# Kernel tuning notes

Hardware: AMD Instinct MI355X
Metric: run time of the kernel (lower is better)

The kernel has to match this reference:

```python
import jax, jax.numpy as jnp
import numpy as np

P = 8192          # pool_size
D = 4096          # input_dim
B = 4             # batch
SPARSITY = 0.1
NC = int(P * P * SPARSITY)  # 6710886 COO nonzeros


def setup_inputs() -> dict:
    key = jax.random.key(0)
    ks = jax.random.split(key, 5)
    return {
        "x": jax.random.normal(ks[0], (B, D), dtype=jnp.float32),
        "W_proj": jax.random.normal(ks[1], (P, D), dtype=jnp.float32) / np.float32(np.sqrt(D)),
        "b_proj": jnp.zeros((P,), dtype=jnp.float32),
        "conn_values": jax.random.normal(ks[2], (NC,), dtype=jnp.float32) * 0.1,
        "sparse_state": jnp.zeros((P,), dtype=jnp.float32),
        "conn_rows": jax.random.randint(ks[3], (NC,), 0, P, dtype=jnp.int32),
        "conn_cols": jax.random.randint(ks[4], (NC,), 0, P, dtype=jnp.int32),
    }


def reference(x, W_proj, b_proj, conn_values, sparse_state, conn_rows, conn_cols):
    # input projection: [B, D] @ [D, P] -> [B, P]
    a = x @ W_proj.T + b_proj
    # quantile threshold over all elements of |a| (matches torch.quantile on full tensor)
    thr = jnp.quantile(jnp.abs(a), 1.0 - SPARSITY)
    mask = jnp.abs(a) > thr                     # [B, P]
    # decay old state, then overwrite active entries with row-0 activation
    a0, m0 = a[0], mask[0]                      # [P], [P]
    state = jnp.where(m0, a0, sparse_state * 0.9)
    # sparse COO matvec: recurrent[r] += v * state[c] for each nonzero (r, c, v)
    contrib = conn_values * state[conn_cols]    # [NC]
    recurrent = jax.ops.segment_sum(contrib, conn_rows, num_segments=P)
    # fused state update + exact GELU (torch nn.GELU default)
    new_state = jax.nn.gelu(state + 0.1 * recurrent, approximate=False)
    # BoundedAttractorState scalars
    active_count = m0.sum()
    mean_activity = jnp.where(
        active_count > 0,
        jnp.sum(jnp.where(m0, new_state, 0.0)) / jnp.maximum(active_count, 1).astype(new_state.dtype),
        0.0,
    )
    return new_state, active_count, mean_activity
```

## Files before the change

### kernel.cpp

```cpp
#include <hip/hip_runtime.h>
#include <math.h>

#define PP 8192
#define DD 4096
#define BBATCH 4
#define NTOT (BBATCH * PP)
#define K_LOW 29490
#define NBINS 8192
#define SCALE 1048576.0f
#define INV_SCALE (1.0f / 1048576.0f)
#define LIST_CAP 3072

__device__ __forceinline__ float dot4(float4 w, float4 v) {
  return fmaf(w.x, v.x, fmaf(w.y, v.y, fmaf(w.z, v.z, w.w * v.w)));
}

__global__ __launch_bounds__(256, 4) void gemm_kernel(const float* __restrict__ x,
                                                      const float* __restrict__ W,
                                                      const float* __restrict__ bias,
                                                      float* __restrict__ a,
                                                      unsigned* __restrict__ hist,
                                                      int* __restrict__ rec) {
  if (blockIdx.x < 32) {
    hist[blockIdx.x * 256 + threadIdx.x] = 0u;
  } else if (blockIdx.x < 64) {
    rec[(blockIdx.x - 32) * 256 + threadIdx.x] = 0;
  }
  const int wave = threadIdx.x >> 6;
  const int lane = threadIdx.x & 63;
  const int p0 = blockIdx.x * 8 + wave * 2;
  const float4* __restrict__ W0 = (const float4*)(W + (size_t)p0 * DD);
  const float4* __restrict__ W1 = W0 + (DD / 4);
  const float4* __restrict__ x4 = (const float4*)x;
  double a00 = 0.0, a01 = 0.0, a02 = 0.0, a03 = 0.0;
  double a10 = 0.0, a11 = 0.0, a12 = 0.0, a13 = 0.0;
  #pragma unroll 4
  for (int k = 0; k < 16; ++k) {
    const int i = lane + k * 64;
    float4 w0 = W0[i];
    float4 w1 = W1[i];
    float4 v0 = x4[i];
    float4 v1 = x4[1024 + i];
    float4 v2 = x4[2048 + i];
    float4 v3 = x4[3072 + i];
    a00 += (double)dot4(w0, v0);
    a01 += (double)dot4(w0, v1);
    a02 += (double)dot4(w0, v2);
    a03 += (double)dot4(w0, v3);
    a10 += (double)dot4(w1, v0);
    a11 += (double)dot4(w1, v1);
    a12 += (double)dot4(w1, v2);
    a13 += (double)dot4(w1, v3);
  }
  #pragma unroll
  for (int off = 32; off > 0; off >>= 1) {
    a00 += __shfl_down(a00, off);
    a01 += __shfl_down(a01, off);
    a02 += __shfl_down(a02, off);
    a03 += __shfl_down(a03, off);
    a10 += __shfl_down(a10, off);
    a11 += __shfl_down(a11, off);
    a12 += __shfl_down(a12, off);
    a13 += __shfl_down(a13, off);
  }
  if (lane == 0) {
    float b0 = bias[p0];
    float b1 = bias[p0 + 1];
    a[0 * PP + p0] = (float)a00 + b0;
    a[1 * PP + p0] = (float)a01 + b0;
    a[2 * PP + p0] = (float)a02 + b0;
    a[3 * PP + p0] = (float)a03 + b0;
    a[0 * PP + p0 + 1] = (float)a10 + b1;
    a[1 * PP + p0 + 1] = (float)a11 + b1;
    a[2 * PP + p0 + 1] = (float)a12 + b1;
    a[3 * PP + p0 + 1] = (float)a13 + b1;
  }
}

__global__ __launch_bounds__(1024) void hist_kernel(const float* __restrict__ a,
                                                    unsigned* __restrict__ hist) {
  __shared__ unsigned h[NBINS];
  const int tid = threadIdx.x;
  #pragma unroll
  for (int j = 0; j < NBINS / 1024; ++j) h[tid + j * 1024] = 0u;
  __syncthreads();
  const int base = blockIdx.x * 4096 + tid;
  #pragma unroll
  for (int k = 0; k < 4; ++k) {
    unsigned u = __float_as_uint(fabsf(a[base + k * 1024]));
    atomicAdd(&h[u >> 18], 1u);
  }
  __syncthreads();
  #pragma unroll
  for (int j = 0; j < NBINS / 1024; ++j) {
    unsigned c = h[tid + j * 1024];
    if (c) atomicAdd(&hist[tid + j * 1024], c);
  }
}

__global__ __launch_bounds__(1024) void thr_kernel(const float* __restrict__ a,
                                                   const unsigned* __restrict__ hist,
                                                   float* __restrict__ thr) {
  __shared__ unsigned scan[1024];
  __shared__ unsigned list1[LIST_CAP];
  __shared__ unsigned list2[LIST_CAP];
  __shared__ unsigned s_n1, s_n2;
  __shared__ unsigned s_b1, s_r1, s_b2, s_r2;
  __shared__ unsigned s_vlo, s_vhi;
  const int tid = threadIdx.x;
  const uint4* h4 = (const uint4*)hist;
  uint4 q0 = h4[tid * 2];
  uint4 q1 = h4[tid * 2 + 1];
  unsigned part = q0.x + q0.y + q0.z + q0.w + q1.x + q1.y + q1.z + q1.w;
  scan[tid] = part;
  if (tid == 0) { s_n1 = 0; s_n2 = 0; }
  __syncthreads();
  for (int off = 1; off < 1024; off <<= 1) {
    unsigned v = (tid >= off) ? scan[tid - off] : 0u;
    __syncthreads();
    scan[tid] += v;
    __syncthreads();
  }
  const unsigned incl = scan[tid];
  const unsigned excl = incl - part;
  unsigned bins[8] = {q0.x, q0.y, q0.z, q0.w, q1.x, q1.y, q1.z, q1.w};
  if (excl <= (unsigned)K_LOW && (unsigned)K_LOW < incl) {
    unsigned r = (unsigned)K_LOW - excl, cum = 0;
    #pragma unroll
    for (int j = 0; j < 8; ++j) {
      if (cum + bins[j] > r) { s_b1 = tid * 8 + j; s_r1 = r - cum; break; }
      cum += bins[j];
    }
  }
  if (excl <= (unsigned)(K_LOW + 1) && (unsigned)(K_LOW + 1) < incl) {
    unsigned r = (unsigned)(K_LOW + 1) - excl, cum = 0;
    #pragma unroll
    for (int j = 0; j < 8; ++j) {
      if (cum + bins[j] > r) { s_b2 = tid * 8 + j; s_r2 = r - cum; break; }
      cum += bins[j];
    }
  }
  __syncthreads();
  const unsigned b1 = s_b1, r1 = s_r1, b2 = s_b2, r2 = s_r2;
  for (int i = tid; i < NTOT; i += 1024) {
    unsigned u = __float_as_uint(fabsf(a[i]));
    unsigned bk = u >> 18;
    if (bk == b1) {
      unsigned idx = atomicAdd(&s_n1, 1u);
      if (idx < LIST_CAP) list1[idx] = u;
    } else if (bk == b2) {
      unsigned idx = atomicAdd(&s_n2, 1u);
      if (idx < LIST_CAP) list2[idx] = u;
    }
  }
  __syncthreads();
  const unsigned m1 = min(s_n1, (unsigned)LIST_CAP);
  const unsigned m2 = min(s_n2, (unsigned)LIST_CAP);
  for (unsigned i = tid; i < m1; i += 1024) {
    unsigned ui = list1[i];
    unsigned ltc = 0, eqb = 0;
    for (unsigned j = 0; j < m1; ++j) {
      unsigned uj = list1[j];
      ltc += (uj < ui) ? 1u : 0u;
      eqb += ((uj == ui) && (j < i)) ? 1u : 0u;
    }
    unsigned rk = ltc + eqb;
    if (rk == r1) s_vlo = ui;
    if (b2 == b1 && rk == r2) s_vhi = ui;
  }
  if (b2 != b1) {
    for (unsigned i = tid; i < m2; i += 1024) {
      unsigned ui = list2[i];
      unsigned ltc = 0, eqb = 0;
      for (unsigned j = 0; j < m2; ++j) {
        unsigned uj = list2[j];
        ltc += (uj < ui) ? 1u : 0u;
        eqb += ((uj == ui) && (j < i)) ? 1u : 0u;
      }
      if (ltc + eqb == r2) s_vhi = ui;
    }
  }
  __syncthreads();
  if (tid == 0) {
    double dlo = (double)__uint_as_float(s_vlo);
    double dhi = (double)__uint_as_float(s_vhi);
    double idx = 0.9 * (double)(NTOT - 1);
    double g = idx - floor(idx);
    thr[0] = (float)(dlo + g * (dhi - dlo));
  }
}

__global__ __launch_bounds__(1024) void spmv_kernel(const float* __restrict__ vals,
                                                    const int* __restrict__ rows,
                                                    const int* __restrict__ cols,
                                                    const float* __restrict__ a,
                                                    const float* __restrict__ thr,
                                                    const float* __restrict__ sstate,
                                                    int* __restrict__ rec,
                                                    int nc) {
  __shared__ float s_state[PP];
  __shared__ int s_rec[PP];
  const int tid = threadIdx.x;
  const float t = thr[0];
  for (int i = tid; i < PP; i += 1024) {
    float a0 = a[i];
    s_state[i] = (fabsf(a0) > t) ? a0 : 0.9f * sstate[i];
    s_rec[i] = 0;
  }
  __syncthreads();
  const int n4 = nc >> 2;
  const int stride = gridDim.x * 1024;
  const float4* __restrict__ v4 = (const float4*)vals;
  const int4* __restrict__ r4 = (const int4*)rows;
  const int4* __restrict__ c4 = (const int4*)cols;
  for (int i = blockIdx.x * 1024 + tid; i < n4; i += stride) {
    float4 v = v4[i];
    int4 r = r4[i];
    int4 c = c4[i];
    atomicAdd((unsigned*)&s_rec[r.x], (unsigned)__float2int_rn(v.x * s_state[c.x] * SCALE));
    atomicAdd((unsigned*)&s_rec[r.y], (unsigned)__float2int_rn(v.y * s_state[c.y] * SCALE));
    atomicAdd((unsigned*)&s_rec[r.z], (unsigned)__float2int_rn(v.z * s_state[c.z] * SCALE));
    atomicAdd((unsigned*)&s_rec[r.w], (unsigned)__float2int_rn(v.w * s_state[c.w] * SCALE));
  }
  if (blockIdx.x == 0 && tid < (nc - (n4 << 2))) {
    int i = (n4 << 2) + tid;
    atomicAdd((unsigned*)&s_rec[rows[i]],
              (unsigned)__float2int_rn(vals[i] * s_state[cols[i]] * SCALE));
  }
  __syncthreads();
  for (int i = tid; i < PP; i += 1024)
    atomicAdd((unsigned*)&rec[i], (unsigned)s_rec[i]);
}

__global__ __launch_bounds__(256) void reduce_gelu_kernel(const int* __restrict__ rec,
                                                          const float* __restrict__ a,
                                                          const float* __restrict__ thr,
                                                          const float* __restrict__ sstate,
                                                          float* __restrict__ out) {
  const int p = blockIdx.x * 256 + threadIdx.x;
  float r = (float)rec[p] * INV_SCALE;
  float a0 = a[p];
  float t = thr[0];
  float st = (fabsf(a0) > t) ? a0 : 0.9f * sstate[p];
  float v = st + 0.1f * r;
  out[p] = 0.5f * v * (1.0f + erff(v * 0.70710678118654752440f));
}

__global__ __launch_bounds__(1024) void scalars_kernel(const float* __restrict__ a,
                                                       const float* __restrict__ thr,
                                                       const float* __restrict__ out_state,
                                                       float* __restrict__ out) {
  __shared__ float wsum[16];
  __shared__ unsigned wcnt[16];
  const float t = thr[0];
  float lsum = 0.0f;
  unsigned lcnt = 0;
  for (int p = threadIdx.x; p < PP; p += 1024) {
    if (fabsf(a[p]) > t) { lsum += out_state[p]; lcnt++; }
  }
  #pragma unroll
  for (int off = 32; off > 0; off >>= 1) {
    lsum += __shfl_down(lsum, off);
    lcnt += __shfl_down(lcnt, off);
  }
  const int lane = threadIdx.x & 63;
  const int wid = threadIdx.x >> 6;
  if (lane == 0) { wsum[wid] = lsum; wcnt[wid] = lcnt; }
  __syncthreads();
  if (threadIdx.x == 0) {
    float s = 0.0f;
    unsigned c = 0;
    for (int w = 0; w < 16; ++w) { s += wsum[w]; c += wcnt[w]; }
    out[PP] = (float)c;
    out[PP + 1] = (c > 0) ? (s / (float)c) : 0.0f;
  }
}

extern "C" void kernel_launch(void* const* d_in, const int* in_sizes, int n_in,
                              void* d_out, int out_size, void* d_ws, size_t ws_size,
                              hipStream_t stream) {
  const float* x      = (const float*)d_in[0];
  const float* W      = (const float*)d_in[1];
  const float* bias   = (const float*)d_in[2];
  const float* vals   = (const float*)d_in[3];
  const float* sstate = (const float*)d_in[4];
  const int*   rows   = (const int*)d_in[5];
  const int*   cols   = (const int*)d_in[6];
  const int    nc     = in_sizes[3];
  float* out = (float*)d_out;
  float* ws  = (float*)d_ws;

  float*    a    = ws;
  float*    thr  = ws + 32768;
  unsigned* hist = (unsigned*)(ws + 32784);
  int*      rec  = (int*)(ws + 32784 + NBINS);

  gemm_kernel<<<PP / 8, 256, 0, stream>>>(x, W, bias, a, hist, rec);
  hist_kernel<<<NTOT / 4096, 1024, 0, stream>>>(a, hist);
  thr_kernel<<<1, 1024, 0, stream>>>(a, hist, thr);
  spmv_kernel<<<256, 1024, 0, stream>>>(vals, rows, cols, a, thr, sstate, rec, nc);
  reduce_gelu_kernel<<<PP / 256, 256, 0, stream>>>(rec, a, thr, sstate, out);
  scalars_kernel<<<1, 1024, 0, stream>>>(a, thr, out, out);
}
```

Before: 82.19 us.

## Fuse histogram into threshold kernel, scalars into GELU, widen GEMM row tile

Removes the multi-block histogram kernel by having the single-block threshold kernel build the histogram in shared memory directly. The scalars reduction is fused into the GELU finalize kernel using fixed-point atomics and a last-block-done counter. The GEMM now computes four rows per wave instead of two, halving the grid. Together these cut two launches, at the cost of a serial 32K-element histogram pass in one block and fixed-point rounding of the mean.

```diff
diff --git a/kernel.cpp b/kernel.cpp
--- a/kernel.cpp
+++ b/kernel.cpp
@@ -3,12 +3,13 @@
 
 #define PP 8192
 #define DD 4096
-#define BBATCH 4
-#define NTOT (BBATCH * PP)
+#define NTOT 32768
 #define K_LOW 29490
 #define NBINS 8192
 #define SCALE 1048576.0f
 #define INV_SCALE (1.0f / 1048576.0f)
+#define MSCALE 262144.0f
+#define INV_MSCALE (1.0f / 262144.0f)
 #define LIST_CAP 3072
 
 __device__ __forceinline__ float dot4(float4 w, float4 v) {
@@ -19,88 +20,75 @@
                                                       const float* __restrict__ W,
                                                       const float* __restrict__ bias,
                                                       float* __restrict__ a,
-                                                      unsigned* __restrict__ hist,
-                                                      int* __restrict__ rec) {
+                                                      int* __restrict__ rec,
+                                                      int* __restrict__ acc) {
   if (blockIdx.x < 32) {
-    hist[blockIdx.x * 256 + threadIdx.x] = 0u;
-  } else if (blockIdx.x < 64) {
-    rec[(blockIdx.x - 32) * 256 + threadIdx.x] = 0;
+    rec[blockIdx.x * 256 + threadIdx.x] = 0;
+  } else if (blockIdx.x == 32 && threadIdx.x < 4) {
+    acc[threadIdx.x] = 0;
   }
   const int wave = threadIdx.x >> 6;
   const int lane = threadIdx.x & 63;
-  const int p0 = blockIdx.x * 8 + wave * 2;
-  const float4* __restrict__ W0 = (const float4*)(W + (size_t)p0 * DD);
-  const float4* __restrict__ W1 = W0 + (DD / 4);
+  const int p0 = blockIdx.x * 16 + wave * 4;
+  const float4* __restrict__ Wr[4];
+  #pragma unroll
+  for (int r = 0; r < 4; ++r) Wr[r] = (const float4*)(W + (size_t)(p0 + r) * DD);
   const float4* __restrict__ x4 = (const float4*)x;
-  double a00 = 0.0, a01 = 0.0, a02 = 0.0, a03 = 0.0;
-  double a10 = 0.0, a11 = 0.0, a12 = 0.0, a13 = 0.0;
-  #pragma unroll 4
+  double accd[4][4];
+  #pragma unroll
+  for (int r = 0; r < 4; ++r)
+    #pragma unroll
+    for (int b = 0; b < 4; ++b) accd[r][b] = 0.0;
+  #pragma unroll 2
   for (int k = 0; k < 16; ++k) {
     const int i = lane + k * 64;
-    float4 w0 = W0[i];
-    float4 w1 = W1[i];
+    float4 w0 = Wr[0][i];
+    float4 w1 = Wr[1][i];
+    float4 w2 = Wr[2][i];
+    float4 w3 = Wr[3][i];
     float4 v0 = x4[i];
     float4 v1 = x4[1024 + i];
     float4 v2 = x4[2048 + i];
     float4 v3 = x4[3072 + i];
-    a00 += (double)dot4(w0, v0);
-    a01 += (double)dot4(w0, v1);
-    a02 += (double)dot4(w0, v2);
-    a03 += (double)dot4(w0, v3);
-    a10 += (double)dot4(w1, v0);
-    a11 += (double)dot4(w1, v1);
-    a12 += (double)dot4(w1, v2);
-    a13 += (double)dot4(w1, v3);
-  }
-  #pragma unroll
-  for (int off = 32; off > 0; off >>= 1) {
-    a00 += __shfl_down(a00, off);
-    a01 += __shfl_down(a01, off);
-    a02 += __shfl_down(a02, off);
-    a03 += __shfl_down(a03, off);
-    a10 += __shfl_down(a10, off);
-    a11 += __shfl_down(a11, off);
-    a12 += __shfl_down(a12, off);
-    a13 += __shfl_down(a13, off);
+    accd[0][0] += (double)dot4(w0, v0);
+    accd[0][1] += (double)dot4(w0, v1);
+    accd[0][2] += (double)dot4(w0, v2);
+    accd[0][3] += (double)dot4(w0, v3);
+    accd[1][0] += (double)dot4(w1, v0);
+    accd[1][1] += (double)dot4(w1, v1);
+    accd[1][2] += (double)dot4(w1, v2);
+    accd[1][3] += (double)dot4(w1, v3);
+    accd[2][0] += (double)dot4(w2, v0);
+    accd[2][1] += (double)dot4(w2, v1);
+    accd[2][2] += (double)dot4(w2, v2);
+    accd[2][3] += (double)dot4(w2, v3);
+    accd[3][0] += (double)dot4(w3, v0);
+    accd[3][1] += (double)dot4(w3, v1);
+    accd[3][2] += (double)dot4(w3, v2);
+    accd[3][3] += (double)dot4(w3, v3);
+  }
+  #pragma unroll
+  for (int r = 0; r < 4; ++r)
+    #pragma unroll
+    for (int b = 0; b < 4; ++b)
+      #pragma unroll
+      for (int off = 32; off > 0; off >>= 1)
+        accd[r][b] += __shfl_down(accd[r][b], off);
+  if (lane < 4) {
   }
   if (lane == 0) {
-    float b0 = bias[p0];
-    float b1 = bias[p0 + 1];
-    a[0 * PP + p0] = (float)a00 + b0;
-    a[1 * PP + p0] = (float)a01 + b0;
-    a[2 * PP + p0] = (float)a02 + b0;
-    a[3 * PP + p0] = (float)a03 + b0;
-    a[0 * PP + p0 + 1] = (float)a10 + b1;
-    a[1 * PP + p0 + 1] = (float)a11 + b1;
-    a[2 * PP + p0 + 1] = (float)a12 + b1;
-    a[3 * PP + p0 + 1] = (float)a13 + b1;
-  }
-}
-
-__global__ __launch_bounds__(1024) void hist_kernel(const float* __restrict__ a,
-                                                    unsigned* __restrict__ hist) {
+    #pragma unroll
+    for (int r = 0; r < 4; ++r) {
+      float bp = bias[p0 + r];
+      #pragma unroll
+      for (int b = 0; b < 4; ++b) a[b * PP + p0 + r] = (float)accd[r][b] + bp;
+    }
+  }
+}
+
+__global__ __launch_bounds__(1024) void thr_kernel(const float* __restrict__ a,
+                                                   float* __restrict__ thr) {
   __shared__ unsigned h[NBINS];
-  const int tid = threadIdx.x;
-  #pragma unroll
-  for (int j = 0; j < NBINS / 1024; ++j) h[tid + j * 1024] = 0u;
-  __syncthreads();
-  const int base = blockIdx.x * 4096 + tid;
-  #pragma unroll
-  for (int k = 0; k < 4; ++k) {
-    unsigned u = __float_as_uint(fabsf(a[base + k * 1024]));
-    atomicAdd(&h[u >> 18], 1u);
-  }
-  __syncthreads();
-  #pragma unroll
-  for (int j = 0; j < NBINS / 1024; ++j) {
-    unsigned c = h[tid + j * 1024];
-    if (c) atomicAdd(&hist[tid + j * 1024], c);
-  }
-}
-
-__global__ __launch_bounds__(1024) void thr_kernel(const float* __restrict__ a,
-                                                   const unsigned* __restrict__ hist,
-                                                   float* __restrict__ thr) {
   __shared__ unsigned scan[1024];
   __shared__ unsigned list1[LIST_CAP];
   __shared__ unsigned list2[LIST_CAP];
@@ -108,12 +96,22 @@
   __shared__ unsigned s_b1, s_r1, s_b2, s_r2;
   __shared__ unsigned s_vlo, s_vhi;
   const int tid = threadIdx.x;
-  const uint4* h4 = (const uint4*)hist;
-  uint4 q0 = h4[tid * 2];
-  uint4 q1 = h4[tid * 2 + 1];
-  unsigned part = q0.x + q0.y + q0.z + q0.w + q1.x + q1.y + q1.z + q1.w;
+  #pragma unroll
+  for (int j = 0; j < NBINS / 1024; ++j) h[tid + j * 1024] = 0u;
+  if (tid == 0) { s_n1 = 0; s_n2 = 0; }
+  __syncthreads();
+  for (int i = tid; i < NTOT; i += 1024) {
+    unsigned u = __float_as_uint(fabsf(a[i]));
+    atomicAdd(&h[u >> 18], 1u);
+  }
+  __syncthreads();
+  unsigned bins[8];
+  #pragma unroll
+  for (int j = 0; j < 8; ++j) bins[j] = h[tid * 8 + j];
+  unsigned part = 0;
+  #pragma unroll
+  for (int j = 0; j < 8; ++j) part += bins[j];
   scan[tid] = part;
-  if (tid == 0) { s_n1 = 0; s_n2 = 0; }
   __syncthreads();
   for (int off = 1; off < 1024; off <<= 1) {
     unsigned v = (tid >= off) ? scan[tid - off] : 0u;
@@ -123,7 +121,6 @@
   }
   const unsigned incl = scan[tid];
   const unsigned excl = incl - part;
-  unsigned bins[8] = {q0.x, q0.y, q0.z, q0.w, q1.x, q1.y, q1.z, q1.w};
   if (excl <= (unsigned)K_LOW && (unsigned)K_LOW < incl) {
     unsigned r = (unsigned)K_LOW - excl, cum = 0;
     #pragma unroll
@@ -232,32 +229,25 @@
     atomicAdd((unsigned*)&rec[i], (unsigned)s_rec[i]);
 }
 
-__global__ __launch_bounds__(256) void reduce_gelu_kernel(const int* __restrict__ rec,
-                                                          const float* __restrict__ a,
-                                                          const float* __restrict__ thr,
-                                                          const float* __restrict__ sstate,
-                                                          float* __restrict__ out) {
+__global__ __launch_bounds__(256) void finalize_kernel(const int* __restrict__ rec,
+                                                       const float* __restrict__ a,
+                                                       const float* __restrict__ thr,
+                                                       const float* __restrict__ sstate,
+                                                       float* __restrict__ out,
+                                                       int* __restrict__ acc) {
+  __shared__ float wsum[4];
+  __shared__ unsigned wcnt[4];
   const int p = blockIdx.x * 256 + threadIdx.x;
+  const float t = thr[0];
   float r = (float)rec[p] * INV_SCALE;
   float a0 = a[p];
-  float t = thr[0];
   float st = (fabsf(a0) > t) ? a0 : 0.9f * sstate[p];
   float v = st + 0.1f * r;
-  out[p] = 0.5f * v * (1.0f + erff(v * 0.70710678118654752440f));
-}
-
-__global__ __launch_bounds__(1024) void scalars_kernel(const float* __restrict__ a,
-                                                       const float* __restrict__ thr,
-                                                       const float* __restrict__ out_state,
-                                                       float* __restrict__ out) {
-  __shared__ float wsum[16];
-  __shared__ unsigned wcnt[16];
-  const float t = thr[0];
-  float lsum = 0.0f;
-  unsigned lcnt = 0;
-  for (int p = threadIdx.x; p < PP; p += 1024) {
-    if (fabsf(a[p]) > t) { lsum += out_state[p]; lcnt++; }
-  }
+  float ns = 0.5f * v * (1.0f + erff(v * 0.70710678118654752440f));
+  out[p] = ns;
+  bool m = fabsf(a0) > t;
+  float lsum = m ? ns : 0.0f;
+  unsigned lcnt = m ? 1u : 0u;
   #pragma unroll
   for (int off = 32; off > 0; off >>= 1) {
     lsum += __shfl_down(lsum, off);
@@ -268,11 +258,18 @@
   if (lane == 0) { wsum[wid] = lsum; wcnt[wid] = lcnt; }
   __syncthreads();
   if (threadIdx.x == 0) {
-    float s = 0.0f;
-    unsigned c = 0;
-    for (int w = 0; w < 16; ++w) { s += wsum[w]; c += wcnt[w]; }
-    out[PP] = (float)c;
-    out[PP + 1] = (c > 0) ? (s / (float)c) : 0.0f;
+    float bsum = wsum[0] + wsum[1] + wsum[2] + wsum[3];
+    unsigned bcnt = wcnt[0] + wcnt[1] + wcnt[2] + wcnt[3];
+    atomicAdd((unsigned*)&acc[0], (unsigned)__float2int_rn(bsum * MSCALE));
+    atomicAdd((unsigned*)&acc[1], bcnt);
+    __threadfence();
+    unsigned d = atomicAdd((unsigned*)&acc[2], 1u);
+    if (d == (unsigned)(gridDim.x - 1)) {
+      int sfix = atomicAdd(&acc[0], 0);
+      int cnt = atomicAdd(&acc[1], 0);
+      out[PP] = (float)cnt;
+      out[PP + 1] = (cnt > 0) ? ((float)sfix * INV_MSCALE / (float)cnt) : 0.0f;
+    }
   }
 }
 
@@ -290,15 +287,13 @@
   float* out = (float*)d_out;
   float* ws  = (float*)d_ws;
 
-  float*    a    = ws;
-  float*    thr  = ws + 32768;
-  unsigned* hist = (unsigned*)(ws + 32784);
-  int*      rec  = (int*)(ws + 32784 + NBINS);
-
-  gemm_kernel<<<PP / 8, 256, 0, stream>>>(x, W, bias, a, hist, rec);
-  hist_kernel<<<NTOT / 4096, 1024, 0, stream>>>(a, hist);
-  thr_kernel<<<1, 1024, 0, stream>>>(a, hist, thr);
+  float* a   = ws;
+  float* thr = ws + 32768;
+  int*   rec = (int*)(ws + 32784);
+  int*   acc = (int*)(ws + 32784 + PP);
+
+  gemm_kernel<<<PP / 16, 256, 0, stream>>>(x, W, bias, a, rec, acc);
+  thr_kernel<<<1, 1024, 0, stream>>>(a, thr);
   spmv_kernel<<<256, 1024, 0, stream>>>(vals, rows, cols, a, thr, sstate, rec, nc);
-  reduce_gelu_kernel<<<PP / 256, 256, 0, stream>>>(rec, a, thr, sstate, out);
-  scalars_kernel<<<1, 1024, 0, stream>>>(a, thr, out, out);
-}
+  finalize_kernel<<<PP / 256, 256, 0, stream>>>(rec, a, thr, sstate, out, acc);
+}
```

Measured after the change: 85.06 us. +3.5%, slower.

## Fuse histogram into GEMM epilogue and merge GELU with scalar reduction

Applied to the files above, without the earlier changes.

The histogram of |a| is now built with global atomics in the GEMM epilogue, which removes the separate hist kernel. The GELU kernel and the single-block scalars kernel are merged into one finalize kernel. It does a last-block-done reduction using fixed-point atomics for the sum. Zeroing of hist, rec and acc moves from GEMM blocks to a hipMemsetAsync. This cuts two kernel launches and one reread of a. In exchange it adds contended global atomics on the histogram and a fixed-point approximation of the mean sum.

```diff
diff --git a/kernel.cpp b/kernel.cpp
--- a/kernel.cpp
+++ b/kernel.cpp
@@ -3,12 +3,13 @@
 
 #define PP 8192
 #define DD 4096
-#define BBATCH 4
-#define NTOT (BBATCH * PP)
+#define NTOT 32768
 #define K_LOW 29490
 #define NBINS 8192
 #define SCALE 1048576.0f
 #define INV_SCALE (1.0f / 1048576.0f)
+#define MSCALE 262144.0f
+#define INV_MSCALE (1.0f / 262144.0f)
 #define LIST_CAP 3072
 
 __device__ __forceinline__ float dot4(float4 w, float4 v) {
@@ -19,13 +20,7 @@
                                                       const float* __restrict__ W,
                                                       const float* __restrict__ bias,
                                                       float* __restrict__ a,
-                                                      unsigned* __restrict__ hist,
-                                                      int* __restrict__ rec) {
-  if (blockIdx.x < 32) {
-    hist[blockIdx.x * 256 + threadIdx.x] = 0u;
-  } else if (blockIdx.x < 64) {
-    rec[(blockIdx.x - 32) * 256 + threadIdx.x] = 0;
-  }
+                                                      unsigned* __restrict__ hist) {
   const int wave = threadIdx.x >> 6;
   const int lane = threadIdx.x & 63;
   const int p0 = blockIdx.x * 8 + wave * 2;
@@ -66,35 +61,30 @@
   if (lane == 0) {
     float b0 = bias[p0];
     float b1 = bias[p0 + 1];
-    a[0 * PP + p0] = (float)a00 + b0;
-    a[1 * PP + p0] = (float)a01 + b0;
-    a[2 * PP + p0] = (float)a02 + b0;
-    a[3 * PP + p0] = (float)a03 + b0;
-    a[0 * PP + p0 + 1] = (float)a10 + b1;
-    a[1 * PP + p0 + 1] = (float)a11 + b1;
-    a[2 * PP + p0 + 1] = (float)a12 + b1;
-    a[3 * PP + p0 + 1] = (float)a13 + b1;
-  }
-}
-
-__global__ __launch_bounds__(1024) void hist_kernel(const float* __restrict__ a,
-                                                    unsigned* __restrict__ hist) {
-  __shared__ unsigned h[NBINS];
-  const int tid = threadIdx.x;
-  #pragma unroll
-  for (int j = 0; j < NBINS / 1024; ++j) h[tid + j * 1024] = 0u;
-  __syncthreads();
-  const int base = blockIdx.x * 4096 + tid;
-  #pragma unroll
-  for (int k = 0; k < 4; ++k) {
-    unsigned u = __float_as_uint(fabsf(a[base + k * 1024]));
-    atomicAdd(&h[u >> 18], 1u);
-  }
-  __syncthreads();
-  #pragma unroll
-  for (int j = 0; j < NBINS / 1024; ++j) {
-    unsigned c = h[tid + j * 1024];
-    if (c) atomicAdd(&hist[tid + j * 1024], c);
+    float r00 = (float)a00 + b0;
+    float r01 = (float)a01 + b0;
+    float r02 = (float)a02 + b0;
+    float r03 = (float)a03 + b0;
+    float r10 = (float)a10 + b1;
+    float r11 = (float)a11 + b1;
+    float r12 = (float)a12 + b1;
+    float r13 = (float)a13 + b1;
+    a[0 * PP + p0] = r00;
+    a[1 * PP + p0] = r01;
+    a[2 * PP + p0] = r02;
+    a[3 * PP + p0] = r03;
+    a[0 * PP + p0 + 1] = r10;
+    a[1 * PP + p0 + 1] = r11;
+    a[2 * PP + p0 + 1] = r12;
+    a[3 * PP + p0 + 1] = r13;
+    atomicAdd(&hist[__float_as_uint(fabsf(r00)) >> 18], 1u);
+    atomicAdd(&hist[__float_as_uint(fabsf(r01)) >> 18], 1u);
+    atomicAdd(&hist[__float_as_uint(fabsf(r02)) >> 18], 1u);
+    atomicAdd(&hist[__float_as_uint(fabsf(r03)) >> 18], 1u);
+    atomicAdd(&hist[__float_as_uint(fabsf(r10)) >> 18], 1u);
+    atomicAdd(&hist[__float_as_uint(fabsf(r11)) >> 18], 1u);
+    atomicAdd(&hist[__float_as_uint(fabsf(r12)) >> 18], 1u);
+    atomicAdd(&hist[__float_as_uint(fabsf(r13)) >> 18], 1u);
   }
 }
 
@@ -232,32 +222,25 @@
     atomicAdd((unsigned*)&rec[i], (unsigned)s_rec[i]);
 }
 
-__global__ __launch_bounds__(256) void reduce_gelu_kernel(const int* __restrict__ rec,
-                                                          const float* __restrict__ a,
-                                                          const float* __restrict__ thr,
-                                                          const float* __restrict__ sstate,
-                                                          float* __restrict__ out) {
+__global__ __launch_bounds__(256) void finalize_kernel(const int* __restrict__ rec,
+                                                       const float* __restrict__ a,
+                                                       const float* __restrict__ thr,
+                                                       const float* __restrict__ sstate,
+                                                       float* __restrict__ out,
+                                                       int* __restrict__ acc) {
+  __shared__ float wsum[4];
+  __shared__ unsigned wcnt[4];
   const int p = blockIdx.x * 256 + threadIdx.x;
+  const float t = thr[0];
   float r = (float)rec[p] * INV_SCALE;
   float a0 = a[p];
-  float t = thr[0];
-  float st = (fabsf(a0) > t) ? a0 : 0.9f * sstate[p];
+  bool m = fabsf(a0) > t;
+  float st = m ? a0 : 0.9f * sstate[p];
   float v = st + 0.1f * r;
-  out[p] = 0.5f * v * (1.0f + erff(v * 0.70710678118654752440f));
-}
-
-__global__ __launch_bounds__(1024) void scalars_kernel(const float* __restrict__ a,
-                                                       const float* __restrict__ thr,
-                                                       const float* __restrict__ out_state,
-                                                       float* __restrict__ out) {
-  __shared__ float wsum[16];
-  __shared__ unsigned wcnt[16];
-  const float t = thr[0];
-  float lsum = 0.0f;
-  unsigned lcnt = 0;
-  for (int p = threadIdx.x; p < PP; p += 1024) {
-    if (fabsf(a[p]) > t) { lsum += out_state[p]; lcnt++; }
-  }
+  float ns = 0.5f * v * (1.0f + erff(v * 0.70710678118654752440f));
+  out[p] = ns;
+  float lsum = m ? ns : 0.0f;
+  unsigned lcnt = m ? 1u : 0u;
   #pragma unroll
   for (int off = 32; off > 0; off >>= 1) {
     lsum += __shfl_down(lsum, off);
@@ -268,11 +251,18 @@
   if (lane == 0) { wsum[wid] = lsum; wcnt[wid] = lcnt; }
   __syncthreads();
   if (threadIdx.x == 0) {
-    float s = 0.0f;
-    unsigned c = 0;
-    for (int w = 0; w < 16; ++w) { s += wsum[w]; c += wcnt[w]; }
-    out[PP] = (float)c;
-    out[PP + 1] = (c > 0) ? (s / (float)c) : 0.0f;
+    float bsum = wsum[0] + wsum[1] + wsum[2] + wsum[3];
+    unsigned bcnt = wcnt[0] + wcnt[1] + wcnt[2] + wcnt[3];
+    atomicAdd((unsigned*)&acc[0], (unsigned)__float2int_rn(bsum * MSCALE));
+    atomicAdd((unsigned*)&acc[1], bcnt);
+    __threadfence();
+    unsigned d = atomicAdd((unsigned*)&acc[2], 1u);
+    if (d == (unsigned)(gridDim.x - 1)) {
+      int sfix = (int)atomicAdd((unsigned*)&acc[0], 0u);
+      int cnt = (int)atomicAdd((unsigned*)&acc[1], 0u);
+      out[PP] = (float)cnt;
+      out[PP + 1] = (cnt > 0) ? ((float)sfix * INV_MSCALE / (float)cnt) : 0.0f;
+    }
   }
 }
 
@@ -294,11 +284,11 @@
   float*    thr  = ws + 32768;
   unsigned* hist = (unsigned*)(ws + 32784);
   int*      rec  = (int*)(ws + 32784 + NBINS);
-
-  gemm_kernel<<<PP / 8, 256, 0, stream>>>(x, W, bias, a, hist, rec);
-  hist_kernel<<<NTOT / 4096, 1024, 0, stream>>>(a, hist);
+  int*      acc  = (int*)(ws + 32784 + NBINS + PP);
+
+  hipMemsetAsync(hist, 0, (NBINS + PP + 4) * sizeof(unsigned), stream);
+  gemm_kernel<<<PP / 8, 256, 0, stream>>>(x, W, bias, a, hist);
   thr_kernel<<<1, 1024, 0, stream>>>(a, hist, thr);
   spmv_kernel<<<256, 1024, 0, stream>>>(vals, rows, cols, a, thr, sstate, rec, nc);
-  reduce_gelu_kernel<<<PP / 256, 256, 0, stream>>>(rec, a, thr, sstate, out);
-  scalars_kernel<<<1, 1024, 0, stream>>>(a, thr, out, out);
-}
+  finalize_kernel<<<PP / 256, 256, 0, stream>>>(rec, a, thr, sstate, out, acc);
+}
```

New measurement: 162.9 us. 98.2% more time.
